# Kernel tuning notes

Hardware: AMD Instinct MI355X
Metric: run time of the kernel (lower is better)

Reference implementation:

```python
import jax, jax.numpy as jnp
import numpy as np

N, M, D, G, E = 1024, 1024, 1024, 16, 64  # rois, ref rois, feat_dim, groups, emb_dim
DG = D // G  # 64 per-group dim


def _make_boxes(k, n):
    k1, k2 = jax.random.split(k)
    xy = jax.random.uniform(k1, (n, 2), dtype=jnp.float32) * 500.0
    wh = jax.random.uniform(k2, (n, 2), dtype=jnp.float32) * 100.0 + 1.0
    return jnp.concatenate([xy, xy + wh], axis=1)  # [n,4] xmin,ymin,xmax,ymax


def setup_inputs() -> dict:
    key = jax.random.key(0)
    ks = jax.random.split(key, 10)
    s = 0.02
    return {
        "roi_feat": jax.random.normal(ks[0], (N, D), dtype=jnp.float32),
        "ref_feat": jax.random.normal(ks[1], (M, D), dtype=jnp.float32),
        "rois1": _make_boxes(ks[2], N),
        "rois2": _make_boxes(ks[3], M),
        "Wq": jax.random.normal(ks[4], (D, D), dtype=jnp.float32) * s,
        "bq": jnp.zeros((D,), jnp.float32),
        "Wk": jax.random.normal(ks[5], (D, D), dtype=jnp.float32) * s,
        "bk": jnp.zeros((D,), jnp.float32),
        "Wg": jax.random.normal(ks[6], (G, E), dtype=jnp.float32) * s,
        "bg": jnp.zeros((G,), jnp.float32),
        "Wv": jax.random.normal(ks[7], (G, DG, D), dtype=jnp.float32) * s,
        "bv": jnp.zeros((D,), jnp.float32),
    }


def _position_matrix(bbox, ref_bbox):
    # bbox [N,4], ref_bbox [M,4] -> [N,M,4]
    def parts(b):
        xmin, ymin, xmax, ymax = b[:, 0], b[:, 1], b[:, 2], b[:, 3]
        w = xmax - xmin + 1.0
        h = ymax - ymin + 1.0
        cx = 0.5 * (xmin + xmax)
        cy = 0.5 * (ymin + ymax)
        return w, h, cx, cy

    w, h, cx, cy = parts(bbox)            # [N]
    wr, hr, cxr, cyr = parts(ref_bbox)    # [M]
    dx = jnp.log(jnp.abs((cx[:, None] - cxr[None, :]) / w[:, None]) + 1e-3)
    dy = jnp.log(jnp.abs((cy[:, None] - cyr[None, :]) / h[:, None]) + 1e-3)
    dw = jnp.log(w[:, None] / wr[None, :])
    dh = jnp.log(h[:, None] / hr[None, :])
    return jnp.stack([dx, dy, dw, dh], axis=2)  # [N,M,4]


def _position_embedding(pos_mat, feat_dim=64, wave_length=1000.0):
    fr = jnp.arange(feat_dim // 8, dtype=jnp.float32)            # [8]
    dim_mat = jnp.power(wave_length, (8.0 / feat_dim) * fr)      # [8]
    div = pos_mat[..., None] * 100.0 / dim_mat                   # [N,M,4,8]
    emb = jnp.concatenate([jnp.sin(div), jnp.cos(div)], axis=3)  # [N,M,4,16]
    return emb.reshape(pos_mat.shape[0], pos_mat.shape[1], -1)   # [N,M,64]


def reference(roi_feat, ref_feat, rois1, rois2, Wq, bq, Wk, bk, Wg, bg, Wv, bv):
    # position embedding: [N,M,E]
    pos_emb = _position_embedding(_position_matrix(rois1, rois2), feat_dim=E)
    # Wgs 1x1 conv (E -> G) + relu -> aff_weight [N,G,M]
    aff_weight = jax.nn.relu(jnp.einsum("nme,ge->ngm", pos_emb, Wg) + bg[None, :, None])
    # grouped q/k projections
    q = (roi_feat @ Wq + bq).reshape(N, G, DG)   # [N,G,dg]
    k = (ref_feat @ Wk + bk).reshape(M, G, DG)   # [M,G,dg]
    aff = jnp.einsum("ngd,mgd->ngm", q, k) * (1.0 / np.sqrt(DG))
    weighted = jnp.log(aff_weight + 1e-6) + aff  # [N,G,M]
    sm = jax.nn.softmax(weighted, axis=2)
    out_t = jnp.einsum("ngm,md->ngd", sm, ref_feat)          # [N,G,D]
    out = jnp.einsum("ngd,god->ngo", out_t, Wv).reshape(N, D) + bv  # grouped 1x1 conv
    return out
```

## Files before the change

### kernel.cpp

```cpp
#include <hip/hip_runtime.h>
#include <hip/hip_fp16.h>
#include <cstddef>

#define N_ 1024
#define M_ 1024
#define D_ 1024
#define G_ 16
#define DG_ 64

typedef __bf16 bf16x8 __attribute__((ext_vector_type(8)));
typedef _Float16 f16x8 __attribute__((ext_vector_type(8)));
typedef float f32x4 __attribute__((ext_vector_type(4)));

__device__ __forceinline__ size_t qkf_idx(int g, int rb, int ks, int lane) {
    return ((((size_t)(g * 64 + rb)) * 2 + ks) * 64 + lane) * 8;
}
__device__ __forceinline__ size_t vf_idx(int g, int ot, int mc, int lane) {
    return ((((size_t)(g * 4 + ot)) * 32 + mc) * 64 + lane) * 8;
}
__device__ __forceinline__ size_t awt_idx(int g, int mb, int n, int quad) {
    return (((size_t)(mb * 1024 + n)) * 16 + g) * 16 + quad * 4;
}

__global__ __launch_bounds__(256)
void fused_mid(const float* __restrict__ roi, const float* __restrict__ ref,
               const float* __restrict__ Wq, const float* __restrict__ Wk,
               const float* __restrict__ Wv,
               const float* __restrict__ bq, const float* __restrict__ bk,
               __bf16* __restrict__ Qf, __bf16* __restrict__ Kf,
               __bf16* __restrict__ Vf,
               const float* __restrict__ rois1, const float* __restrict__ rois2,
               const float* __restrict__ Wg, const float* __restrict__ bg,
               __half* __restrict__ AWt)
{
    __shared__ __align__(16) char smem[36864];
    const int b = blockIdx.x;
    const int tid = threadIdx.x;
    const int w = tid >> 6, lane = tid & 63;
    const int quad = lane >> 4, l15 = lane & 15;

    if (b < 2112 && (b % 11 == 0)) {
        const int t = b / 11;
        const int z = t >> 6, t6 = t & 63;
        const float* A = (z == 0) ? roi : ref;
        const float* Wf = (z == 0) ? Wq : (z == 1) ? Wk : Wv;
        const int i0 = (t6 >> 3) * 128, j0 = (t6 & 7) * 128;
        const int iw = (w & 1) * 64, jw = (w >> 1) * 64;

        __bf16(*As)[72] = (__bf16(*)[72])smem;
        __bf16(*Bs)[72] = (__bf16(*)[72])(smem + 18432);

        f32x4 acc[4][4] = {};

        for (int k0 = 0; k0 < D_; k0 += 64) {
            __syncthreads();
            #pragma unroll
            for (int it = 0; it < 8; ++it) {
                const int idx = tid + 256 * it;
                const int row = idx >> 4, c = idx & 15;
                float4 a = *(const float4*)&A[(size_t)(i0 + row) * D_ + k0 + c * 4];
                __bf16 p[4] = {(__bf16)a.x, (__bf16)a.y, (__bf16)a.z, (__bf16)a.w};
                *(uint2*)&As[row][c * 4] = *(const uint2*)p;
            }
            if (z < 2) {
                #pragma unroll
                for (int it = 0; it < 8; ++it) {
                    const int idx = tid + 256 * it;
                    const int jl = idx & 127;
                    const int kc = idx >> 7;
                    const float* src = &Wf[(size_t)(k0 + kc * 4) * D_ + j0 + jl];
                    __bf16 p[4];
                    p[0] = (__bf16)src[0];
                    p[1] = (__bf16)src[D_];
                    p[2] = (__bf16)src[2 * D_];
                    p[3] = (__bf16)src[3 * D_];
                    *(uint2*)&Bs[jl][kc * 4] = *(const uint2*)p;
                }
            } else {
                #pragma unroll
                for (int it = 0; it < 8; ++it) {
                    const int idx = tid + 256 * it;
                    const int row = idx >> 4, c = idx & 15;
                    float4 a = *(const float4*)&Wf[(size_t)(j0 + row) * D_ + k0 + c * 4];
                    __bf16 p[4] = {(__bf16)a.x, (__bf16)a.y, (__bf16)a.z, (__bf16)a.w};
                    *(uint2*)&Bs[row][c * 4] = *(const uint2*)p;
                }
            }
            __syncthreads();
            #pragma unroll
            for (int ks = 0; ks < 2; ++ks) {
                bf16x8 af[4], bfr[4];
                #pragma unroll
                for (int t4 = 0; t4 < 4; ++t4) {
                    af[t4]  = *(const bf16x8*)&As[iw + t4 * 16 + l15][ks * 32 + quad * 8];
                    bfr[t4] = *(const bf16x8*)&Bs[jw + t4 * 16 + l15][ks * 32 + quad * 8];
                }
                #pragma unroll
                for (int ti = 0; ti < 4; ++ti)
                    #pragma unroll
                    for (int tj = 0; tj < 4; ++tj)
                        acc[ti][tj] = __builtin_amdgcn_mfma_f32_16x16x32_bf16(
                            af[ti], bfr[tj], acc[ti][tj], 0, 0, 0);
            }
        }

        if (z < 2) {
            const float* bias = (z == 0) ? bq : bk;
            __bf16* dst = (z == 0) ? Qf : Kf;
            const float scale = (z == 0) ? 0.125f : 1.0f;
            #pragma unroll
            for (int ti = 0; ti < 4; ++ti) {
                const int rb = (i0 + iw + ti * 16) >> 4;
                #pragma unroll
                for (int tj = 0; tj < 4; ++tj) {
                    const int go = j0 + jw + tj * 16 + l15;
                    const int g = go >> 6, ks = (go >> 5) & 1;
                    const int lanef = ((go >> 3) & 3) * 16;
                    const int jf = go & 7;
                    const float bb = bias[go];
                    __bf16* base = dst + qkf_idx(g, rb, ks, 0) + jf;
                    #pragma unroll
                    for (int r = 0; r < 4; ++r)
                        base[(size_t)(lanef + quad * 4 + r) * 8] =
                            (__bf16)((acc[ti][tj][r] + bb) * scale);
                }
            }
        } else {
            #pragma unroll
            for (int ti = 0; ti < 4; ++ti) {
                const int mbase = i0 + iw + ti * 16 + quad * 4;
                const int mc = mbase >> 5, quadv = (mbase >> 3) & 3, jb = mbase & 7;
                #pragma unroll
                for (int tj = 0; tj < 4; ++tj) {
                    const int go = j0 + jw + tj * 16 + l15;
                    const int g = go >> 6, ot = (go >> 4) & 3, o15 = go & 15;
                    __bf16 p[4];
                    #pragma unroll
                    for (int r = 0; r < 4; ++r) p[r] = (__bf16)acc[ti][tj][r];
                    *(uint2*)&Vf[vf_idx(g, ot, mc, quadv * 16 + o15) + jb] =
                        *(const uint2*)p;
                }
            }
        }
        return;
    }

    const int gcnt_raw = (b + 10) / 11;
    const int pb = b - (gcnt_raw < 192 ? gcnt_raw : 192);
    const int n = pb >> 2;
    const int m0w = (pb & 3) * 256 + w * 64;

    const float xmin = rois1[n * 4 + 0], ymin = rois1[n * 4 + 1];
    const float xmax = rois1[n * 4 + 2], ymax = rois1[n * 4 + 3];
    const float wn  = xmax - xmin + 1.f, hn  = ymax - ymin + 1.f;
    const float cxn = 0.5f * (xmin + xmax), cyn = 0.5f * (ymin + ymax);
    const float rwn = 1.0f / wn, rhn = 1.0f / hn;
    const float lwn = __logf(wn), lhn = __logf(hn);

    f16x8 wgf[2];
    #pragma unroll
    for (int ks = 0; ks < 2; ++ks) {
        const float* p = &Wg[l15 * 64 + ks * 32 + quad * 8];
        float4 a = *(const float4*)p;
        float4 bb = *(const float4*)(p + 4);
        wgf[ks][0] = (_Float16)a.x; wgf[ks][1] = (_Float16)a.y;
        wgf[ks][2] = (_Float16)a.z; wgf[ks][3] = (_Float16)a.w;
        wgf[ks][4] = (_Float16)bb.x; wgf[ks][5] = (_Float16)bb.y;
        wgf[ks][6] = (_Float16)bb.z; wgf[ks][7] = (_Float16)bb.w;
    }
    const float bgv = bg[l15];

    const float fr8[8] = {100.0f, 42.16965f, 17.782794f, 7.4989421f,
                          3.1622777f, 1.3335214f, 0.56234133f, 0.23713737f};
    const float phase = (quad & 1) ? 1.5707963267948966f : 0.f;

    #pragma unroll
    for (int ti = 0; ti < 4; ++ti) {
        const int mt0 = m0w + ti * 16;
        const int m = mt0 + l15;
        float4 r2 = *(const float4*)&rois2[m * 4];
        const float wr  = r2.z - r2.x + 1.f, hr  = r2.w - r2.y + 1.f;
        const float cxr = 0.5f * (r2.x + r2.z), cyr = 0.5f * (r2.y + r2.w);

        const float f0 = __logf(fabsf((cxn - cxr) * rwn) + 0.001f);
        const float f1 = __logf(fabsf((cyn - cyr) * rhn) + 0.001f);
        const float f2 = lwn - __logf(wr);
        const float f3 = lhn - __logf(hr);
        const float fa = (quad & 2) ? f1 : f0;
        const float fb = (quad & 2) ? f3 : f2;

        f32x4 acc = {};
        #pragma unroll
        for (int ks = 0; ks < 2; ++ks) {
            const float feat = ks ? fb : fa;
            f16x8 ef;
            #pragma unroll
            for (int j = 0; j < 8; ++j)
                ef[j] = (_Float16)__sinf(fmaf(feat, fr8[j], phase));
            acc = __builtin_amdgcn_mfma_f32_16x16x32_f16(ef, wgf[ks], acc, 0, 0, 0);
        }

        __half p[4];
        #pragma unroll
        for (int r = 0; r < 4; ++r)
            p[r] = __float2half(fmaxf(acc[r] + bgv, 0.f) + 1e-6f);
        *(uint2*)&AWt[awt_idx(l15, mt0 >> 4, n, quad)] = *(const uint2*)p;
    }
}

__global__ __launch_bounds__(256)
void attn_mfma(const __bf16* __restrict__ Qf, const __bf16* __restrict__ Kf,
               const __bf16* __restrict__ Vf, const __half* __restrict__ AWt,
               const float* __restrict__ bv, float* __restrict__ out)
{
    __shared__ __align__(16) char smem[17664];

    const int tid = threadIdx.x;
    const int w = tid >> 6, lane = tid & 63;
    const int quad = lane >> 4, l15 = lane & 15;
    const int nb = blockIdx.x, n0 = nb * 16, g = blockIdx.y;

    __bf16(*Psw)[72] = (__bf16(*)[72])(smem + w * 2304);
    float(*accb)[64][17] = (float(*)[64][17])smem;
    float(*lsb)[16] = (float(*)[16])(smem + 17408);

    bf16x8 qf[2];
    qf[0] = *(const bf16x8*)&Qf[qkf_idx(g, nb, 0, lane)];
    qf[1] = *(const bf16x8*)&Qf[qkf_idx(g, nb, 1, lane)];

    f32x4 acc[4] = {};
    float llocal = 0.f;

    #pragma unroll
    for (int t64 = 0; t64 < 4; ++t64) {
        const int mt = w * 4 + t64;

        f32x4 s[4];
        #pragma unroll
        for (int t = 0; t < 4; ++t) {
            bf16x8 ka0 = *(const bf16x8*)&Kf[qkf_idx(g, mt * 4 + t, 0, lane)];
            bf16x8 ka1 = *(const bf16x8*)&Kf[qkf_idx(g, mt * 4 + t, 1, lane)];
            f32x4 z = {};
            __builtin_amdgcn_s_setprio(1);
            z = __builtin_amdgcn_mfma_f32_16x16x32_bf16(ka0, qf[0], z, 0, 0, 0);
            s[t] = __builtin_amdgcn_mfma_f32_16x16x32_bf16(ka1, qf[1], z, 0, 0, 0);
            __builtin_amdgcn_s_setprio(0);
        }

        #pragma unroll
        for (int t = 0; t < 4; ++t) {
            uint2 au = *(const uint2*)&AWt[awt_idx(g, mt * 4 + t, n0 + l15, quad)];
            const __half* a4 = (const __half*)&au;
            __bf16 pk[4];
            #pragma unroll
            for (int r = 0; r < 4; ++r) {
                const float p = __half2float(a4[r]) * __expf(s[t][r]);
                llocal += p;
                pk[r] = (__bf16)p;
            }
            *(uint2*)&Psw[l15][t * 16 + quad * 4] = *(const uint2*)pk;
        }

        #pragma unroll
        for (int mcl = 0; mcl < 2; ++mcl) {
            bf16x8 pbf = *(const bf16x8*)&Psw[l15][mcl * 32 + quad * 8];
            __builtin_amdgcn_s_setprio(1);
            #pragma unroll
            for (int ot = 0; ot < 4; ++ot) {
                bf16x8 va = *(const bf16x8*)&Vf[vf_idx(g, ot, mt * 2 + mcl, lane)];
                acc[ot] = __builtin_amdgcn_mfma_f32_16x16x32_bf16(va, pbf, acc[ot], 0, 0, 0);
            }
            __builtin_amdgcn_s_setprio(0);
        }
    }

    llocal += __shfl_xor(llocal, 16, 64);
    llocal += __shfl_xor(llocal, 32, 64);

    __syncthreads();

    #pragma unroll
    for (int ot = 0; ot < 4; ++ot)
        #pragma unroll
        for (int r = 0; r < 4; ++r)
            accb[w][ot * 16 + quad * 4 + r][l15] = acc[ot][r];
    if (quad == 0) lsb[w][l15] = llocal;
    __syncthreads();

    const float lt = lsb[0][l15] + lsb[1][l15] + lsb[2][l15] + lsb[3][l15];
    const float inv = 1.f / lt;
    #pragma unroll
    for (int r = 0; r < 4; ++r) {
        const int o = w * 16 + quad * 4 + r;
        const int ogl = g * 64 + o;
        const float v = accb[0][o][l15] + accb[1][o][l15] +
                        accb[2][o][l15] + accb[3][o][l15];
        out[(size_t)(n0 + l15) * D_ + ogl] = v * inv + bv[ogl];
    }
}

extern "C" void kernel_launch(void* const* d_in, const int* in_sizes, int n_in,
                              void* d_out, int out_size, void* d_ws, size_t ws_size,
                              hipStream_t stream) {
    const float* roi_feat = (const float*)d_in[0];
    const float* ref_feat = (const float*)d_in[1];
    const float* rois1    = (const float*)d_in[2];
    const float* rois2    = (const float*)d_in[3];
    const float* Wq       = (const float*)d_in[4];
    const float* bq       = (const float*)d_in[5];
    const float* Wk       = (const float*)d_in[6];
    const float* bk       = (const float*)d_in[7];
    const float* Wg       = (const float*)d_in[8];
    const float* bg       = (const float*)d_in[9];
    const float* Wv       = (const float*)d_in[10];
    const float* bv       = (const float*)d_in[11];
    float* out = (float*)d_out;

    char* ws = (char*)d_ws;
    __bf16* Qf  = (__bf16*)(ws + 0);
    __bf16* Kf  = (__bf16*)(ws + (2u << 20));
    __bf16* Vf  = (__bf16*)(ws + (4u << 20));
    __half* AWt = (__half*)(ws + (6u << 20));

    dim3 blk(256);
    fused_mid<<<dim3(4288), blk, 0, stream>>>(roi_feat, ref_feat, Wq, Wk, Wv,
                                              bq, bk, Qf, Kf, Vf,
                                              rois1, rois2, Wg, bg, AWt);
    attn_mfma<<<dim3(64, 16), blk, 0, stream>>>(Qf, Kf, Vf, AWt, bv, out);
}
```

Measured before the change: 142.7 us.

## Split fused QKV GEMM and position-bias kernel into separate launches

Replaces the single interleaved kernel that ran the QKV projection GEMM and the position-bias computation in one grid with two sequential kernels. The position-bias kernel now uses one block per roi and loops over all four reference quarters. This removes the block-index dispatch logic and the heterogeneous blocks within one launch. In exchange it loses the concurrent overlap of GEMM and transcendental work and adds a launch boundary.

After: 158.2 us. +10.9%, slower.

```diff
diff --git a/kernel.cpp b/kernel.cpp
--- a/kernel.cpp
+++ b/kernel.cpp
@@ -23,132 +23,131 @@
 }
 
 __global__ __launch_bounds__(256)
-void fused_mid(const float* __restrict__ roi, const float* __restrict__ ref,
-               const float* __restrict__ Wq, const float* __restrict__ Wk,
-               const float* __restrict__ Wv,
-               const float* __restrict__ bq, const float* __restrict__ bk,
-               __bf16* __restrict__ Qf, __bf16* __restrict__ Kf,
-               __bf16* __restrict__ Vf,
-               const float* __restrict__ rois1, const float* __restrict__ rois2,
-               const float* __restrict__ Wg, const float* __restrict__ bg,
-               __half* __restrict__ AWt)
+void gemm_qkv(const float* __restrict__ roi, const float* __restrict__ ref,
+              const float* __restrict__ Wq, const float* __restrict__ Wk,
+              const float* __restrict__ Wv,
+              const float* __restrict__ bq, const float* __restrict__ bk,
+              __bf16* __restrict__ Qf, __bf16* __restrict__ Kf,
+              __bf16* __restrict__ Vf)
 {
     __shared__ __align__(16) char smem[36864];
-    const int b = blockIdx.x;
+    const int t = blockIdx.x;
     const int tid = threadIdx.x;
     const int w = tid >> 6, lane = tid & 63;
     const int quad = lane >> 4, l15 = lane & 15;
 
-    if (b < 2112 && (b % 11 == 0)) {
-        const int t = b / 11;
-        const int z = t >> 6, t6 = t & 63;
-        const float* A = (z == 0) ? roi : ref;
-        const float* Wf = (z == 0) ? Wq : (z == 1) ? Wk : Wv;
-        const int i0 = (t6 >> 3) * 128, j0 = (t6 & 7) * 128;
-        const int iw = (w & 1) * 64, jw = (w >> 1) * 64;
-
-        __bf16(*As)[72] = (__bf16(*)[72])smem;
-        __bf16(*Bs)[72] = (__bf16(*)[72])(smem + 18432);
-
-        f32x4 acc[4][4] = {};
-
-        for (int k0 = 0; k0 < D_; k0 += 64) {
-            __syncthreads();
+    const int z = t >> 6, t6 = t & 63;
+    const float* A = (z == 0) ? roi : ref;
+    const float* Wf = (z == 0) ? Wq : (z == 1) ? Wk : Wv;
+    const int i0 = (t6 >> 3) * 128, j0 = (t6 & 7) * 128;
+    const int iw = (w & 1) * 64, jw = (w >> 1) * 64;
+
+    __bf16(*As)[72] = (__bf16(*)[72])smem;
+    __bf16(*Bs)[72] = (__bf16(*)[72])(smem + 18432);
+
+    f32x4 acc[4][4] = {};
+
+    for (int k0 = 0; k0 < D_; k0 += 64) {
+        __syncthreads();
+        #pragma unroll
+        for (int it = 0; it < 8; ++it) {
+            const int idx = tid + 256 * it;
+            const int row = idx >> 4, c = idx & 15;
+            float4 a = *(const float4*)&A[(size_t)(i0 + row) * D_ + k0 + c * 4];
+            __bf16 p[4] = {(__bf16)a.x, (__bf16)a.y, (__bf16)a.z, (__bf16)a.w};
+            *(uint2*)&As[row][c * 4] = *(const uint2*)p;
+        }
+        if (z < 2) {
+            #pragma unroll
+            for (int it = 0; it < 8; ++it) {
+                const int idx = tid + 256 * it;
+                const int jl = idx & 127;
+                const int kc = idx >> 7;
+                const float* src = &Wf[(size_t)(k0 + kc * 4) * D_ + j0 + jl];
+                __bf16 p[4];
+                p[0] = (__bf16)src[0];
+                p[1] = (__bf16)src[D_];
+                p[2] = (__bf16)src[2 * D_];
+                p[3] = (__bf16)src[3 * D_];
+                *(uint2*)&Bs[jl][kc * 4] = *(const uint2*)p;
+            }
+        } else {
             #pragma unroll
             for (int it = 0; it < 8; ++it) {
                 const int idx = tid + 256 * it;
                 const int row = idx >> 4, c = idx & 15;
-                float4 a = *(const float4*)&A[(size_t)(i0 + row) * D_ + k0 + c * 4];
+                float4 a = *(const float4*)&Wf[(size_t)(j0 + row) * D_ + k0 + c * 4];
                 __bf16 p[4] = {(__bf16)a.x, (__bf16)a.y, (__bf16)a.z, (__bf16)a.w};
-                *(uint2*)&As[row][c * 4] = *(const uint2*)p;
-            }
-            if (z < 2) {
+                *(uint2*)&Bs[row][c * 4] = *(const uint2*)p;
+            }
+        }
+        __syncthreads();
+        #pragma unroll
+        for (int ks = 0; ks < 2; ++ks) {
+            bf16x8 af[4], bfr[4];
+            #pragma unroll
+            for (int t4 = 0; t4 < 4; ++t4) {
+                af[t4]  = *(const bf16x8*)&As[iw + t4 * 16 + l15][ks * 32 + quad * 8];
+                bfr[t4] = *(const bf16x8*)&Bs[jw + t4 * 16 + l15][ks * 32 + quad * 8];
+            }
+            #pragma unroll
+            for (int ti = 0; ti < 4; ++ti)
                 #pragma unroll
-                for (int it = 0; it < 8; ++it) {
-                    const int idx = tid + 256 * it;
-                    const int jl = idx & 127;
-                    const int kc = idx >> 7;
-                    const float* src = &Wf[(size_t)(k0 + kc * 4) * D_ + j0 + jl];
-                    __bf16 p[4];
-                    p[0] = (__bf16)src[0];
-                    p[1] = (__bf16)src[D_];
-                    p[2] = (__bf16)src[2 * D_];
-                    p[3] = (__bf16)src[3 * D_];
-                    *(uint2*)&Bs[jl][kc * 4] = *(const uint2*)p;
-                }
-            } else {
+                for (int tj = 0; tj < 4; ++tj)
+                    acc[ti][tj] = __builtin_amdgcn_mfma_f32_16x16x32_bf16(
+                        af[ti], bfr[tj], acc[ti][tj], 0, 0, 0);
+        }
+    }
+
+    if (z < 2) {
+        const float* bias = (z == 0) ? bq : bk;
+        __bf16* dst = (z == 0) ? Qf : Kf;
+        const float scale = (z == 0) ? 0.125f : 1.0f;
+        #pragma unroll
+        for (int ti = 0; ti < 4; ++ti) {
+            const int rb = (i0 + iw + ti * 16) >> 4;
+            #pragma unroll
+            for (int tj = 0; tj < 4; ++tj) {
+                const int go = j0 + jw + tj * 16 + l15;
+                const int g = go >> 6, ks = (go >> 5) & 1;
+                const int lanef = ((go >> 3) & 3) * 16;
+                const int jf = go & 7;
+                const float bb = bias[go];
+                __bf16* base = dst + qkf_idx(g, rb, ks, 0) + jf;
                 #pragma unroll
-                for (int it = 0; it < 8; ++it) {
-                    const int idx = tid + 256 * it;
-                    const int row = idx >> 4, c = idx & 15;
-                    float4 a = *(const float4*)&Wf[(size_t)(j0 + row) * D_ + k0 + c * 4];
-                    __bf16 p[4] = {(__bf16)a.x, (__bf16)a.y, (__bf16)a.z, (__bf16)a.w};
-                    *(uint2*)&Bs[row][c * 4] = *(const uint2*)p;
-                }
-            }
-            __syncthreads();
-            #pragma unroll
-            for (int ks = 0; ks < 2; ++ks) {
-                bf16x8 af[4], bfr[4];
+                for (int r = 0; r < 4; ++r)
+                    base[(size_t)(lanef + quad * 4 + r) * 8] =
+                        (__bf16)((acc[ti][tj][r] + bb) * scale);
+            }
+        }
+    } else {
+        #pragma unroll
+        for (int ti = 0; ti < 4; ++ti) {
+            const int mbase = i0 + iw + ti * 16 + quad * 4;
+            const int mc = mbase >> 5, quadv = (mbase >> 3) & 3, jb = mbase & 7;
+            #pragma unroll
+            for (int tj = 0; tj < 4; ++tj) {
+                const int go = j0 + jw + tj * 16 + l15;
+                const int g = go >> 6, ot = (go >> 4) & 3, o15 = go & 15;
+                __bf16 p[4];
                 #pragma unroll
-                for (int t4 = 0; t4 < 4; ++t4) {
-                    af[t4]  = *(const bf16x8*)&As[iw + t4 * 16 + l15][ks * 32 + quad * 8];
-                    bfr[t4] = *(const bf16x8*)&Bs[jw + t4 * 16 + l15][ks * 32 + quad * 8];
-                }
-                #pragma unroll
-                for (int ti = 0; ti < 4; ++ti)
-                    #pragma unroll
-                    for (int tj = 0; tj < 4; ++tj)
-                        acc[ti][tj] = __builtin_amdgcn_mfma_f32_16x16x32_bf16(
-                            af[ti], bfr[tj], acc[ti][tj], 0, 0, 0);
-            }
-        }
-
-        if (z < 2) {
-            const float* bias = (z == 0) ? bq : bk;
-            __bf16* dst = (z == 0) ? Qf : Kf;
-            const float scale = (z == 0) ? 0.125f : 1.0f;
-            #pragma unroll
-            for (int ti = 0; ti < 4; ++ti) {
-                const int rb = (i0 + iw + ti * 16) >> 4;
-                #pragma unroll
-                for (int tj = 0; tj < 4; ++tj) {
-                    const int go = j0 + jw + tj * 16 + l15;
-                    const int g = go >> 6, ks = (go >> 5) & 1;
-                    const int lanef = ((go >> 3) & 3) * 16;
-                    const int jf = go & 7;
-                    const float bb = bias[go];
-                    __bf16* base = dst + qkf_idx(g, rb, ks, 0) + jf;
-                    #pragma unroll
-                    for (int r = 0; r < 4; ++r)
-                        base[(size_t)(lanef + quad * 4 + r) * 8] =
-                            (__bf16)((acc[ti][tj][r] + bb) * scale);
-                }
-            }
-        } else {
-            #pragma unroll
-            for (int ti = 0; ti < 4; ++ti) {
-                const int mbase = i0 + iw + ti * 16 + quad * 4;
-                const int mc = mbase >> 5, quadv = (mbase >> 3) & 3, jb = mbase & 7;
-                #pragma unroll
-                for (int tj = 0; tj < 4; ++tj) {
-                    const int go = j0 + jw + tj * 16 + l15;
-                    const int g = go >> 6, ot = (go >> 4) & 3, o15 = go & 15;
-                    __bf16 p[4];
-                    #pragma unroll
-                    for (int r = 0; r < 4; ++r) p[r] = (__bf16)acc[ti][tj][r];
-                    *(uint2*)&Vf[vf_idx(g, ot, mc, quadv * 16 + o15) + jb] =
-                        *(const uint2*)p;
-                }
-            }
-        }
-        return;
-    }
-
-    const int gcnt_raw = (b + 10) / 11;
-    const int pb = b - (gcnt_raw < 192 ? gcnt_raw : 192);
-    const int n = pb >> 2;
-    const int m0w = (pb & 3) * 256 + w * 64;
+                for (int r = 0; r < 4; ++r) p[r] = (__bf16)acc[ti][tj][r];
+                *(uint2*)&Vf[vf_idx(g, ot, mc, quadv * 16 + o15) + jb] =
+                    *(const uint2*)p;
+            }
+        }
+    }
+}
+
+__global__ __launch_bounds__(256)
+void posbias(const float* __restrict__ rois1, const float* __restrict__ rois2,
+             const float* __restrict__ Wg, const float* __restrict__ bg,
+             __half* __restrict__ AWt)
+{
+    const int tid = threadIdx.x;
+    const int w = tid >> 6, lane = tid & 63;
+    const int quad = lane >> 4, l15 = lane & 15;
+    const int n = blockIdx.x;
 
     const float xmin = rois1[n * 4 + 0], ymin = rois1[n * 4 + 1];
     const float xmax = rois1[n * 4 + 2], ymax = rois1[n * 4 + 3];
@@ -174,37 +173,40 @@
                           3.1622777f, 1.3335214f, 0.56234133f, 0.23713737f};
     const float phase = (quad & 1) ? 1.5707963267948966f : 0.f;
 
-    #pragma unroll
-    for (int ti = 0; ti < 4; ++ti) {
-        const int mt0 = m0w + ti * 16;
-        const int m = mt0 + l15;
-        float4 r2 = *(const float4*)&rois2[m * 4];
-        const float wr  = r2.z - r2.x + 1.f, hr  = r2.w - r2.y + 1.f;
-        const float cxr = 0.5f * (r2.x + r2.z), cyr = 0.5f * (r2.y + r2.w);
-
-        const float f0 = __logf(fabsf((cxn - cxr) * rwn) + 0.001f);
-        const float f1 = __logf(fabsf((cyn - cyr) * rhn) + 0.001f);
-        const float f2 = lwn - __logf(wr);
-        const float f3 = lhn - __logf(hr);
-        const float fa = (quad & 2) ? f1 : f0;
-        const float fb = (quad & 2) ? f3 : f2;
-
-        f32x4 acc = {};
-        #pragma unroll
-        for (int ks = 0; ks < 2; ++ks) {
-            const float feat = ks ? fb : fa;
-            f16x8 ef;
-            #pragma unroll
-            for (int j = 0; j < 8; ++j)
-                ef[j] = (_Float16)__sinf(fmaf(feat, fr8[j], phase));
-            acc = __builtin_amdgcn_mfma_f32_16x16x32_f16(ef, wgf[ks], acc, 0, 0, 0);
-        }
-
-        __half p[4];
-        #pragma unroll
-        for (int r = 0; r < 4; ++r)
-            p[r] = __float2half(fmaxf(acc[r] + bgv, 0.f) + 1e-6f);
-        *(uint2*)&AWt[awt_idx(l15, mt0 >> 4, n, quad)] = *(const uint2*)p;
+    for (int mq = 0; mq < 4; ++mq) {
+        const int m0w = mq * 256 + w * 64;
+        #pragma unroll
+        for (int ti = 0; ti < 4; ++ti) {
+            const int mt0 = m0w + ti * 16;
+            const int m = mt0 + l15;
+            float4 r2 = *(const float4*)&rois2[m * 4];
+            const float wr  = r2.z - r2.x + 1.f, hr  = r2.w - r2.y + 1.f;
+            const float cxr = 0.5f * (r2.x + r2.z), cyr = 0.5f * (r2.y + r2.w);
+
+            const float f0 = __logf(fabsf((cxn - cxr) * rwn) + 0.001f);
+            const float f1 = __logf(fabsf((cyn - cyr) * rhn) + 0.001f);
+            const float f2 = lwn - __logf(wr);
+            const float f3 = lhn - __logf(hr);
+            const float fa = (quad & 2) ? f1 : f0;
+            const float fb = (quad & 2) ? f3 : f2;
+
+            f32x4 acc = {};
+            #pragma unroll
+            for (int ks = 0; ks < 2; ++ks) {
+                const float feat = ks ? fb : fa;
+                f16x8 ef;
+                #pragma unroll
+                for (int j = 0; j < 8; ++j)
+                    ef[j] = (_Float16)__sinf(fmaf(feat, fr8[j], phase));
+                acc = __builtin_amdgcn_mfma_f32_16x16x32_f16(ef, wgf[ks], acc, 0, 0, 0);
+            }
+
+            __half p[4];
+            #pragma unroll
+            for (int r = 0; r < 4; ++r)
+                p[r] = __float2half(fmaxf(acc[r] + bgv, 0.f) + 1e-6f);
+            *(uint2*)&AWt[awt_idx(l15, mt0 >> 4, n, quad)] = *(const uint2*)p;
+        }
     }
 }
 
@@ -323,8 +325,8 @@
     __half* AWt = (__half*)(ws + (6u << 20));
 
     dim3 blk(256);
-    fused_mid<<<dim3(4288), blk, 0, stream>>>(roi_feat, ref_feat, Wq, Wk, Wv,
-                                              bq, bk, Qf, Kf, Vf,
-                                              rois1, rois2, Wg, bg, AWt);
+    gemm_qkv<<<dim3(192), blk, 0, stream>>>(roi_feat, ref_feat, Wq, Wk, Wv,
+                                            bq, bk, Qf, Kf, Vf);
+    posbias<<<dim3(1024), blk, 0, stream>>>(rois1, rois2, Wg, bg, AWt);
     attn_mfma<<<dim3(64, 16), blk, 0, stream>>>(Qf, Kf, Vf, AWt, bv, out);
 }
```
